# Kernel optimization log

Hardware: AMD Instinct MI355X
Metric: run time of the kernel (lower is better)

## Reference

```python
import jax, jax.numpy as jnp
import numpy as np

B = 8192
NUM_NETS, N_NODES, NUM_OUT, DIM_OUT = 30, 20, 10, 16
NUM_ITER = 3
IN_DIM = 28 * 28


def squash(t, axis=-1):
    # scale * t / ||t||, scale = ||t||^2 / (1 + ||t||^2)
    sq = jnp.sum(t * t, axis=axis, keepdims=True)
    return (sq / (1.0 + sq)) * t / jnp.sqrt(sq)


def setup_inputs() -> dict:
    key = jax.random.key(0)
    ks = jax.random.split(key, 6)
    return {
        "x": jax.random.normal(ks[0], (B, IN_DIM), dtype=jnp.float32),
        "W1": jax.random.normal(ks[1], (NUM_NETS, IN_DIM, N_NODES), dtype=jnp.float32) * 0.05,
        "b1": jax.random.normal(ks[2], (NUM_NETS, N_NODES), dtype=jnp.float32) * 0.05,
        "W2": jax.random.normal(ks[3], (NUM_NETS, N_NODES, N_NODES), dtype=jnp.float32) * 0.05,
        "b2": jax.random.normal(ks[4], (NUM_NETS, N_NODES), dtype=jnp.float32) * 0.05,
        "route_weights": jax.random.normal(ks[5], (NUM_OUT, NUM_NETS, N_NODES, DIM_OUT), dtype=jnp.float32),
    }


def reference(x, W1, b1, W2, b2, route_weights):
    # 30 independent MLPs batched into one grouped GEMM each
    h = jax.nn.relu(jnp.einsum("bi,nio->bno", x, W1) + b1)          # [B,N,20]
    h = jax.nn.relu(jnp.einsum("bnd,nde->bne", h, W2) + b2)          # [B,N,20]
    u = squash(h, axis=-1)                                            # per-net squash over features
    # priors[b,o,n,k] = sum_d u[b,n,d] * route_weights[o,n,d,k]
    priors = jnp.einsum("bnd,ondk->bonk", u, route_weights)          # [B,O,N,K]
    # logits are constant along K in the original; keep [B,O,N,1] (exact math)
    logits = jnp.zeros(priors.shape[:3] + (1,), dtype=priors.dtype)
    v = None
    for i in range(NUM_ITER):
        probs = jax.nn.softmax(logits, axis=1)                        # over output capsules
        v = squash(jnp.sum(probs * priors, axis=2, keepdims=True))    # [B,O,1,K]
        if i != NUM_ITER - 1:
            logits = logits + jnp.sum(priors * v, axis=-1, keepdims=True)
    return jnp.squeeze(v, axis=2)                                     # [B,O,K]
```

## Files before the change

### kernel.cpp

```cpp
#include <hip/hip_runtime.h>


typedef unsigned short bfu;
typedef unsigned int u32;
typedef __attribute__((ext_vector_type(8))) short short8;
typedef __attribute__((ext_vector_type(4))) float floatx4;

__device__ __forceinline__ float bf2f(bfu u) { union { u32 i; float f; } v; v.i = ((u32)u) << 16; return v.f; }
__device__ __forceinline__ float lo2f(u32 w) { union { u32 i; float f; } v; v.i = w << 16; return v.f; }
__device__ __forceinline__ float hi2f(u32 w) { union { u32 i; float f; } v; v.i = w & 0xffff0000u; return v.f; }
__device__ __forceinline__ float ldf(const void* p, int idx, bool b16) {
    return b16 ? bf2f(((const bfu*)p)[idx]) : ((const float*)p)[idx];
}
__device__ __forceinline__ bfu f2bf(float f) {
    u32 u = __float_as_uint(f);
    return (bfu)((u + 0x7FFFu + ((u >> 16) & 1u)) >> 16);
}
__device__ __forceinline__ void unpack8(uint4 q, float* dst) {
    dst[0] = lo2f(q.x); dst[1] = hi2f(q.x);
    dst[2] = lo2f(q.y); dst[3] = hi2f(q.y);
    dst[4] = lo2f(q.z); dst[5] = hi2f(q.z);
    dst[6] = lo2f(q.w); dst[7] = hi2f(q.w);
}

__global__ void detect_dtype(const u32* x, const u32* W1, const u32* b1,
                             const u32* W2, const u32* b2, const u32* rw,
                             u32* flags) {
    int t = threadIdx.x;
    if (t >= 6) return;
    const u32* p = (t == 0) ? x : (t == 1) ? W1 : (t == 2) ? b1
                 : (t == 3) ? W2 : (t == 4) ? b2 : rw;
    int c = 0;
    for (int i = 0; i < 64; i++) {
        u32 e = (p[i] >> 7) & 0xFF;
        c += (e >= 64 && e <= 140) ? 1 : 0;
    }
    flags[t] = (c >= 48) ? 1u : 0u;
}

__global__ void prep_all(const void* x, const void* W1, const void* b1,
                         const void* W2, const void* b2, const void* rw,
                         bfu* __restrict__ xb, bfu* __restrict__ Wt,
                         float* __restrict__ b1f, bfu* __restrict__ rwb,
                         bfu* __restrict__ rwn, float* __restrict__ W2t,
                         float* __restrict__ b2f,
                         const u32* flags, int B, int mode) {
    const int idx = blockIdx.x * 256 + threadIdx.x;
    const int nxb = B * 800;
    if (idx < nxb) {
        const bool b16 = flags[0] != 0;
        int b = idx / 800, kk = idx - b * 800;
        bfu v = 0;
        if (kk < 784) {
            int src = b * 784 + kk;
            v = b16 ? ((const bfu*)x)[src] : f2bf(((const float*)x)[src]);
        }
        xb[idx] = v;
        return;
    }
    int i2 = idx - nxb;
    if (i2 < 640 * 800) {
        const bool wb = flags[1] != 0;
        int c = i2 / 800, k = i2 - c * 800;
        bfu v = 0;
        if (c < 600 && k < 784) {
            int nn = c / 20, o = c - nn * 20;
            int src = nn * 15680 + k * 20 + o;
            v = wb ? ((const bfu*)W1)[src] : f2bf(((const float*)W1)[src]);
        }
        Wt[i2] = v;
        return;
    }
    i2 -= 640 * 800;
    if (i2 < 96000) {
        const bool rb = flags[5] != 0;
        int d = i2 % 20;
        int k = (i2 / 20) % 16;
        int n = (i2 / 320) % 30;
        int o = i2 / 9600;
        int src = o * 9600 + n * 320 + d * 16 + k;
        rwb[i2] = rb ? ((const bfu*)rw)[src] : f2bf(((const float*)rw)[src]);
        return;
    }
    i2 -= 96000;
    if (i2 < 640) {
        b1f[i2] = (i2 < 600) ? ldf(b1, i2, flags[2] != 0) : 0.f;
        return;
    }
    i2 -= 640;
    if (mode != 0) return;
    if (i2 < 153600) {
        const bool rb = flags[5] != 0;
        int dd = i2 % 32;
        int col = (i2 / 32) % 160;
        int n = i2 / 5120;
        bfu v = 0;
        if (dd < 20) {
            int o = col / 16, kk = col % 16;
            int src = o * 9600 + n * 320 + dd * 16 + kk;
            v = rb ? ((const bfu*)rw)[src] : f2bf(((const float*)rw)[src]);
        }
        rwn[i2] = v;
        return;
    }
    i2 -= 153600;
    if (i2 < 12000) {
        int d = i2 % 20;
        int e = (i2 / 20) % 20;
        int n = i2 / 400;
        W2t[i2] = ldf(W2, n * 400 + d * 20 + e, flags[3] != 0);
        return;
    }
    i2 -= 12000;
    if (i2 < 640) {
        b2f[i2] = (i2 < 600) ? ldf(b2, i2, flags[4] != 0) : 0.f;
    }
}

__global__ __launch_bounds__(256, 4) void k1m(const bfu* __restrict__ xb, const bfu* __restrict__ Wt,
                                              const float* __restrict__ b1f,
                                              float* __restrict__ h1, int Btot, int tr) {
    __shared__ short As[128 * 40];
    __shared__ short Bs[64 * 40];
    const int tid = threadIdx.x;
    const int w = tid >> 6, lane = tid & 63;
    const int quad = lane >> 4, fl = lane & 15;
    const int m0 = blockIdx.x * 128, n0 = blockIdx.y * 64;

    floatx4 acc[2][4];
    #pragma unroll
    for (int mi = 0; mi < 2; mi++)
        #pragma unroll
        for (int ni = 0; ni < 4; ni++) acc[mi][ni] = (floatx4){0.f, 0.f, 0.f, 0.f};

    const int arow = tid >> 1, aseg = tid & 1;
    const int brow = tid >> 2, bseg = tid & 3;
    int agrow = m0 + arow; if (agrow >= Btot) agrow = Btot - 1;
    const bfu* abase = xb + (size_t)agrow * 800 + aseg * 16;
    const bfu* bbase = Wt + (size_t)(n0 + brow) * 800 + bseg * 8;

    for (int k0 = 0; k0 < 800; k0 += 32) {
        uint4 qa0 = *(const uint4*)(abase + k0);
        uint4 qa1 = *(const uint4*)(abase + k0 + 8);
        uint4 qb  = *(const uint4*)(bbase + k0);

        __syncthreads();
        *(uint4*)&As[arow * 40 + aseg * 16 + 0] = qa0;
        *(uint4*)&As[arow * 40 + aseg * 16 + 8] = qa1;
        *(uint4*)&Bs[brow * 40 + bseg * 8] = qb;
        __syncthreads();

        short8 af[2], bfr[4];
        #pragma unroll
        for (int mi = 0; mi < 2; mi++)
            af[mi] = *(const short8*)&As[(w * 32 + mi * 16 + fl) * 40 + quad * 8];
        #pragma unroll
        for (int ni = 0; ni < 4; ni++)
            bfr[ni] = *(const short8*)&Bs[(ni * 16 + fl) * 40 + quad * 8];
        #pragma unroll
        for (int mi = 0; mi < 2; mi++)
            #pragma unroll
            for (int ni = 0; ni < 4; ni++)
                acc[mi][ni] = __builtin_amdgcn_mfma_f32_16x16x32_bf16(af[mi], bfr[ni], acc[mi][ni], 0, 0, 0);
    }

    #pragma unroll
    for (int mi = 0; mi < 2; mi++) {
        #pragma unroll
        for (int ni = 0; ni < 4; ni++) {
            const int c = n0 + ni * 16 + fl;
            const int cn = c / 20, ce = c - cn * 20;
            #pragma unroll
            for (int r = 0; r < 4; r++) {
                const int m = m0 + w * 32 + mi * 16 + quad * 4 + r;
                if (c < 600 && m < Btot) {
                    size_t di = tr ? (((size_t)cn * Btot + m) * 20 + ce)
                                   : ((size_t)m * 600 + c);
                    h1[di] = fmaxf(acc[mi][ni][r] + b1f[c], 0.f);
                }
            }
        }
    }
}

__global__ __launch_bounds__(256) void k2n(const float* __restrict__ h1n,
                                           const float* __restrict__ W2t,
                                           const float* __restrict__ b2f,
                                           bfu* __restrict__ ub32, int Btot) {
    const int n = blockIdx.y;
    int b = blockIdx.x * 256 + threadIdx.x;
    if (b >= Btot) b = Btot - 1;

    float h[20];
    const float* hp = h1n + ((size_t)n * Btot + b) * 20;
    #pragma unroll
    for (int d4 = 0; d4 < 20; d4 += 4) {
        float4 v = *(const float4*)(hp + d4);
        h[d4] = v.x; h[d4 + 1] = v.y; h[d4 + 2] = v.z; h[d4 + 3] = v.w;
    }

    const float* wn = W2t + n * 400;
    const float* bn = b2f + n * 20;
    float o[20], sq = 0.f;
    #pragma unroll
    for (int e = 0; e < 20; e++) {
        float acc = bn[e];
        #pragma unroll
        for (int d = 0; d < 20; d++) acc += h[d] * wn[e * 20 + d];
        acc = fmaxf(acc, 0.f);
        o[e] = acc;
        sq += acc * acc;
    }
    float sc = (sq > 0.f) ? sqrtf(sq) / (1.f + sq) : 0.f;

    u32 wbuf[16];
    #pragma unroll
    for (int j = 0; j < 10; j++)
        wbuf[j] = (u32)f2bf(o[2 * j] * sc) | ((u32)f2bf(o[2 * j + 1] * sc) << 16);
    #pragma unroll
    for (int j = 10; j < 16; j++) wbuf[j] = 0;
    uint4* dst = (uint4*)(ub32 + ((size_t)b * 30 + n) * 32);
    dst[0] = *(uint4*)&wbuf[0];
    dst[1] = *(uint4*)&wbuf[4];
    dst[2] = *(uint4*)&wbuf[8];
    dst[3] = *(uint4*)&wbuf[12];
}

__device__ __forceinline__ void k2_core(const float* hp, const float* wn, const float* bn,
                                        float* o, float& sc) {
    float h[20];
    #pragma unroll
    for (int d4 = 0; d4 < 20; d4 += 4) {
        float4 v = *(const float4*)(hp + d4);
        h[d4] = v.x; h[d4 + 1] = v.y; h[d4 + 2] = v.z; h[d4 + 3] = v.w;
    }
    float sq = 0.f;
    #pragma unroll
    for (int e = 0; e < 20; e++) {
        float acc = bn[e];
        #pragma unroll
        for (int d = 0; d < 20; d++) acc += h[d] * wn[d * 20 + e];
        acc = fmaxf(acc, 0.f);
        o[e] = acc;
        sq += acc * acc;
    }
    sc = (sq > 0.f) ? sqrtf(sq) / (1.f + sq) : 0.f;
}

__global__ __launch_bounds__(256) void k2s(const float* h1, const void* W2, const void* b2,
                                           float* u, const u32* flags, int total) {
    __shared__ float W2s[12000];
    __shared__ float b2s[600];
    const bool wb = flags[3] != 0, bb = flags[4] != 0;
    const int tid = threadIdx.x;
    for (int i = tid; i < 12000; i += 256) W2s[i] = ldf(W2, i, wb);
    for (int i = tid; i < 600; i += 256) b2s[i] = ldf(b2, i, bb);
    __syncthreads();

    int t = blockIdx.x * 256 + tid;
    if (t >= total) return;
    const int b = t / 30, n = t - b * 30;
    float o[20], sc;
    k2_core(h1 + (size_t)b * 600 + n * 20, &W2s[n * 400], &b2s[n * 20], o, sc);
    float* up = u + (size_t)b * 600 + n * 20;
    #pragma unroll
    for (int e4 = 0; e4 < 20; e4 += 4) {
        float4 v;
        v.x = o[e4] * sc; v.y = o[e4 + 1] * sc; v.z = o[e4 + 2] * sc; v.w = o[e4 + 3] * sc;
        *(float4*)(up + e4) = v;
    }
}

__global__ __launch_bounds__(256) void k2p(const bfu* __restrict__ ub32,
                                           const bfu* __restrict__ rwn,
                                           bfu* __restrict__ pri, int Btot) {
    const int tid = threadIdx.x;
    const int w = tid >> 6, lane = tid & 63;
    const int quad = lane >> 4, fl = lane & 15;
    const int n = blockIdx.y;
    const int b0 = blockIdx.x * 128;

    short8 bfr[10];
    #pragma unroll
    for (int nj = 0; nj < 10; nj++)
        bfr[nj] = *(const short8*)(rwn + ((size_t)n * 160 + nj * 16 + fl) * 32 + quad * 8);

    #pragma unroll
    for (int mi = 0; mi < 2; mi++) {
        int m = b0 + w * 32 + mi * 16 + fl;
        int mc = (m < Btot) ? m : Btot - 1;
        short8 af = *(const short8*)(ub32 + ((size_t)mc * 30 + n) * 32 + quad * 8);
        #pragma unroll
        for (int nj = 0; nj < 10; nj++) {
            floatx4 acc = (floatx4){0.f, 0.f, 0.f, 0.f};
            acc = __builtin_amdgcn_mfma_f32_16x16x32_bf16(af, bfr[nj], acc, 0, 0, 0);
            #pragma unroll
            for (int r = 0; r < 4; r++) {
                int mr = b0 + w * 32 + mi * 16 + quad * 4 + r;
                if (mr < Btot)
                    pri[(size_t)mr * 4800 + n * 160 + nj * 16 + fl] = f2bf(acc[r]);
            }
        }
    }
}

__global__ __launch_bounds__(640, 2) void k3t(const bfu* __restrict__ pri_buf,
                                              float* __restrict__ out, int Btot) {
    __shared__ float L[4][300];
    __shared__ float P[4][300];
    const int tid = threadIdx.x;
    const int g = tid / 160, r = tid - g * 160;
    const int o = r >> 4, j = r & 15;
    const int b0 = blockIdx.x * 4;
    int bb = b0 + g; if (bb >= Btot) bb = Btot - 1;

    const int n0 = 2 * j, n1 = n0 + 1;
    float p0[16], p1[16];
    if (j < 15) {
        const bfu* pb = pri_buf + (size_t)bb * 4800 + (size_t)o * 16;
        uint4 q0 = *(const uint4*)(pb + n0 * 160);
        uint4 q1 = *(const uint4*)(pb + n0 * 160 + 8);
        uint4 q2 = *(const uint4*)(pb + n1 * 160);
        uint4 q3 = *(const uint4*)(pb + n1 * 160 + 8);
        unpack8(q0, p0); unpack8(q1, p0 + 8);
        unpack8(q2, p1); unpack8(q3, p1 + 8);
    } else {
        #pragma unroll
        for (int i = 0; i < 16; i++) { p0[i] = 0.f; p1[i] = 0.f; }
    }

    float L0 = 0.f, L1 = 0.f;
    float v = 0.f;
    #pragma unroll
    for (int it = 0; it < 3; it++) {
        float P0, P1;
        if (it == 0) {
            P0 = 0.1f; P1 = 0.1f;
        } else {
            if (r < 30) {
                float l[10];
                #pragma unroll
                for (int oo = 0; oo < 10; oo++) l[oo] = L[g][r * 10 + oo];
                float mx = l[0];
                #pragma unroll
                for (int oo = 1; oo < 10; oo++) mx = fmaxf(mx, l[oo]);
                float den = 0.f;
                #pragma unroll
                for (int oo = 0; oo < 10; oo++) { l[oo] = __expf(l[oo] - mx); den += l[oo]; }
                float inv = 1.f / den;
                #pragma unroll
                for (int oo = 0; oo < 10; oo++) P[g][r * 10 + oo] = l[oo] * inv;
            }
            __syncthreads();
            P0 = (j < 15) ? P[g][n0 * 10 + o] : 0.f;
            P1 = (j < 15) ? P[g][n1 * 10 + o] : 0.f;
        }

        float t[16];
        #pragma unroll
        for (int i = 0; i < 16; i++) t[i] = P0 * p0[i] + P1 * p1[i];

        #pragma unroll
        for (int i = 0; i < 8; i++) {
            float send = (j & 8) ? t[i] : t[i + 8];
            float recv = __shfl_xor(send, 8, 16);
            t[i] = ((j & 8) ? t[i + 8] : t[i]) + recv;
        }
        #pragma unroll
        for (int i = 0; i < 4; i++) {
            float send = (j & 4) ? t[i] : t[i + 4];
            float recv = __shfl_xor(send, 4, 16);
            t[i] = ((j & 4) ? t[i + 4] : t[i]) + recv;
        }
        #pragma unroll
        for (int i = 0; i < 2; i++) {
            float send = (j & 2) ? t[i] : t[i + 2];
            float recv = __shfl_xor(send, 2, 16);
            t[i] = ((j & 2) ? t[i + 2] : t[i]) + recv;
        }
        {
            float send = (j & 1) ? t[0] : t[1];
            float recv = __shfl_xor(send, 1, 16);
            t[0] = ((j & 1) ? t[1] : t[0]) + recv;
        }
        float s = t[0];

        if (it < 2) {
            float sf[16];
            #pragma unroll
            for (int k = 0; k < 16; k++) sf[k] = __shfl(s, k, 16);
            float q = 0.f;
            #pragma unroll
            for (int k = 0; k < 16; k++) q += sf[k] * sf[k];
            float scale = sqrtf(q) / (1.f + q);
            v = s * scale;
            float d0 = 0.f, d1 = 0.f;
            #pragma unroll
            for (int k = 0; k < 16; k++) {
                float vk = sf[k] * scale;
                d0 += p0[k] * vk;
                d1 += p1[k] * vk;
            }
            L0 += d0; L1 += d1;
            if (j < 15) {
                L[g][n0 * 10 + o] = L0;
                L[g][n1 * 10 + o] = L1;
            }
            __syncthreads();
        } else {
            float q = s * s;
            q += __shfl_xor(q, 1, 16);
            q += __shfl_xor(q, 2, 16);
            q += __shfl_xor(q, 4, 16);
            q += __shfl_xor(q, 8, 16);
            v = s * sqrtf(q) / (1.f + q);
        }
    }
    if ((b0 + g) < Btot) out[(size_t)(b0 + g) * 160 + r] = v;
}

__global__ __launch_bounds__(640, 2) void k3y2(const float* __restrict__ u,
                                               const bfu* __restrict__ rwb,
                                               float* __restrict__ out, int Btot) {
    __shared__ float US[4][600];
    __shared__ float L[4][300];
    __shared__ float P[4][300];
    const int tid = threadIdx.x;
    const int g = tid / 160, r = tid - g * 160;
    const int o = r >> 4, k = r & 15;
    const int b0 = blockIdx.x * 4;

    {
        const int nf4 = 150;
        for (int i = tid; i < 4 * nf4; i += 640) {
            int gg = i / nf4, j = i - gg * nf4;
            int bb = b0 + gg; if (bb >= Btot) bb = Btot - 1;
            *(float4*)&US[gg][j * 4] = *(const float4*)(u + (size_t)bb * 600 + j * 4);
        }
        for (int i = tid; i < 1200; i += 640) L[i / 300][i % 300] = 0.f;
    }
    __syncthreads();

    float pri[30];
    const bfu* rp = rwb + o * 9600 + k * 20;
    #pragma unroll 2
    for (int n = 0; n < 30; n++) {
        const uint2* rq = (const uint2*)(rp + n * 320);
        float a = 0.f;
        #pragma unroll
        for (int jj = 0; jj < 5; jj++) {
            uint2 w = rq[jj];
            float4 uu = *(const float4*)&US[g][n * 20 + jj * 4];
            a += lo2f(w.x) * uu.x + hi2f(w.x) * uu.y + lo2f(w.y) * uu.z + hi2f(w.y) * uu.w;
        }
        pri[n] = a;
    }

    float v = 0.f;
    for (int it = 0; it < 3; it++) {
        if (r < 30) {
            const int n = r;
            float mx = L[g][n * 10];
            #pragma unroll
            for (int oo = 1; oo < 10; oo++) mx = fmaxf(mx, L[g][n * 10 + oo]);
            float e[10], den = 0.f;
            #pragma unroll
            for (int oo = 0; oo < 10; oo++) { e[oo] = __expf(L[g][n * 10 + oo] - mx); den += e[oo]; }
            float inv = 1.f / den;
            #pragma unroll
            for (int oo = 0; oo < 10; oo++) P[g][n * 10 + oo] = e[oo] * inv;
        }
        __syncthreads();
        float s = 0.f;
        #pragma unroll
        for (int n = 0; n < 30; n++) s += P[g][n * 10 + o] * pri[n];
        float q = s * s;
        q += __shfl_xor(q, 1, 16);
        q += __shfl_xor(q, 2, 16);
        q += __shfl_xor(q, 4, 16);
        q += __shfl_xor(q, 8, 16);
        v = s * sqrtf(q) / (1.f + q);
        if (it < 2) {
            #pragma unroll 5
            for (int n = 0; n < 30; n++) {
                float t = pri[n] * v;
                t += __shfl_xor(t, 1, 16);
                t += __shfl_xor(t, 2, 16);
                t += __shfl_xor(t, 4, 16);
                t += __shfl_xor(t, 8, 16);
                if (k == 0) L[g][n * 10 + o] += t;
            }
            __syncthreads();
        }
    }
    if ((b0 + g) < Btot) out[(size_t)(b0 + g) * 160 + r] = v;
}

extern "C" void kernel_launch(void* const* d_in, const int* in_sizes, int n_in,
                              void* d_out, int out_size, void* d_ws, size_t ws_size,
                              hipStream_t stream) {
    int ix = -1, iw1 = -1, ib1 = -1, iw2 = -1, ib2 = -1, irw = -1;
    for (int i = 0; i < n_in; i++) {
        int s = in_sizes[i];
        if (s == 470400 && iw1 < 0) iw1 = i;
        else if (s == 12000 && iw2 < 0) iw2 = i;
        else if (s == 96000 && irw < 0) irw = i;
        else if (s == 600) { if (ib1 < 0) ib1 = i; else if (ib2 < 0) ib2 = i; }
    }
    long bestsz = -1;
    for (int i = 0; i < n_in; i++) {
        if (i == iw1 || i == iw2 || i == irw || i == ib1 || i == ib2) continue;
        if ((long)in_sizes[i] > bestsz) { bestsz = in_sizes[i]; ix = i; }
    }
    if (ix < 0 || iw1 < 0 || ib1 < 0 || iw2 < 0 || ib2 < 0 || irw < 0) {
        ix = 0; iw1 = 1; ib1 = 2; iw2 = 3; ib2 = 4; irw = 5;
    }
    const void* x  = d_in[ix];
    const void* W1 = d_in[iw1];
    const void* b1 = d_in[ib1];
    const void* W2 = d_in[iw2];
    const void* b2 = d_in[ib2];
    const void* rw = d_in[irw];
    const int B = in_sizes[ix] / 784;
    float* out = (float*)d_out;

    char* base = (char*)d_ws;
    size_t off = 0;
    float* h1u  = (float*)(base + off); off += (size_t)B * 2400;
    float* b1f  = (float*)(base + off); off += 2560;
    u32*  flags = (u32*)(base + off);   off += 32;
    bfu*   Wt   = (bfu*)(base + off);   off += 1024000;
    bfu*   xb   = (bfu*)(base + off);   off += (size_t)B * 1600;
    bfu*   rwb  = (bfu*)(base + off);   off += 192000;
    size_t fb_bytes = off;
    bfu*   rwn  = (bfu*)(base + off);   off += 307200;
    float* W2t  = (float*)(base + off); off += 48000;
    float* b2f  = (float*)(base + off); off += 2560;
    bfu*   ub32 = (bfu*)(base + off);   off += (size_t)B * 1920;
    bfu*   pri  = (bfu*)(base + off);   off += (size_t)B * 9600;
    size_t main_bytes = off;

    const int mode = (ws_size >= main_bytes) ? 0 : 1;
    const int prep_total = B * 800 + 640 * 800 + 96000 + 640
                         + (mode == 0 ? (153600 + 12000 + 640) : 0);

    detect_dtype<<<1, 64, 0, stream>>>((const u32*)x, (const u32*)W1, (const u32*)b1,
                                       (const u32*)W2, (const u32*)b2, (const u32*)rw, flags);
    prep_all<<<(prep_total + 255) / 256, 256, 0, stream>>>(x, W1, b1, W2, b2, rw,
                                                           xb, Wt, b1f, rwb, rwn,
                                                           W2t, b2f, flags, B, mode);
    k1m<<<dim3((B + 127) / 128, 10), 256, 0, stream>>>(xb, Wt, b1f, h1u, B, mode == 0 ? 1 : 0);
    if (mode == 0) {
        k2n<<<dim3((B + 255) / 256, 30), 256, 0, stream>>>(h1u, W2t, b2f, ub32, B);
        k2p<<<dim3((B + 127) / 128, 30), 256, 0, stream>>>(ub32, rwn, pri, B);
        k3t<<<(B + 3) / 4, 640, 0, stream>>>(pri, out, B);
    } else {
        (void)fb_bytes;
        k2s<<<(B * 30 + 255) / 256, 256, 0, stream>>>(h1u, W2, b2, h1u, flags, B * 30);
        k3y2<<<(B + 3) / 4, 640, 0, stream>>>(h1u, rwb, out, B);
    }
}
```

Measured before the change: 191.4 us.

## Reorder priors layout to [o][n][k] and halve routing kernel threads

The prior-producing kernel now writes priors grouped by output capsule first, so each routing thread loads four contiguous nets' 16-wide vectors. The routing kernel uses 80 threads per batch row instead of 160, with each thread handling 4 nets and 2 output dims. This cuts the shuffle reduction depth and idle lanes, and gives vectorized float2 stores. The cost is more registers per thread and fewer threads per block.

Result: no change. 191.1 us (-0.1%).

```diff
diff --git a/kernel.cpp b/kernel.cpp
--- a/kernel.cpp
+++ b/kernel.cpp
@@ -298,44 +298,45 @@
             for (int r = 0; r < 4; r++) {
                 int mr = b0 + w * 32 + mi * 16 + quad * 4 + r;
                 if (mr < Btot)
-                    pri[(size_t)mr * 4800 + n * 160 + nj * 16 + fl] = f2bf(acc[r]);
-            }
-        }
-    }
-}
-
-__global__ __launch_bounds__(640, 2) void k3t(const bfu* __restrict__ pri_buf,
-                                              float* __restrict__ out, int Btot) {
+                    pri[(size_t)mr * 4800 + nj * 480 + n * 16 + fl] = f2bf(acc[r]);
+            }
+        }
+    }
+}
+
+__global__ __launch_bounds__(320) void k3u(const bfu* __restrict__ pri_buf,
+                                           float* __restrict__ out, int Btot) {
     __shared__ float L[4][300];
     __shared__ float P[4][300];
     const int tid = threadIdx.x;
-    const int g = tid / 160, r = tid - g * 160;
-    const int o = r >> 4, j = r & 15;
+    const int g = tid / 80, r = tid - g * 80;
+    const int o = r >> 3, j = r & 7;
     const int b0 = blockIdx.x * 4;
     int bb = b0 + g; if (bb >= Btot) bb = Btot - 1;
 
-    const int n0 = 2 * j, n1 = n0 + 1;
-    float p0[16], p1[16];
-    if (j < 15) {
-        const bfu* pb = pri_buf + (size_t)bb * 4800 + (size_t)o * 16;
-        uint4 q0 = *(const uint4*)(pb + n0 * 160);
-        uint4 q1 = *(const uint4*)(pb + n0 * 160 + 8);
-        uint4 q2 = *(const uint4*)(pb + n1 * 160);
-        uint4 q3 = *(const uint4*)(pb + n1 * 160 + 8);
-        unpack8(q0, p0); unpack8(q1, p0 + 8);
-        unpack8(q2, p1); unpack8(q3, p1 + 8);
-    } else {
-        #pragma unroll
-        for (int i = 0; i < 16; i++) { p0[i] = 0.f; p1[i] = 0.f; }
-    }
-
-    float L0 = 0.f, L1 = 0.f;
-    float v = 0.f;
+    float p[4][16];
+    const bfu* pb = pri_buf + (size_t)bb * 4800 + (size_t)o * 480 + j * 64;
+    #pragma unroll
+    for (int nn = 0; nn < 4; nn++) {
+        if (4 * j + nn < 30) {
+            uint4 q0 = *(const uint4*)(pb + nn * 16);
+            uint4 q1 = *(const uint4*)(pb + nn * 16 + 8);
+            unpack8(q0, p[nn]); unpack8(q1, p[nn] + 8);
+        } else {
+            #pragma unroll
+            for (int i = 0; i < 16; i++) p[nn][i] = 0.f;
+        }
+    }
+
+    float Lr[4] = {0.f, 0.f, 0.f, 0.f};
+    float v0 = 0.f, v1 = 0.f;
     #pragma unroll
     for (int it = 0; it < 3; it++) {
-        float P0, P1;
+        float t[16];
         if (it == 0) {
-            P0 = 0.1f; P1 = 0.1f;
+            #pragma unroll
+            for (int i = 0; i < 16; i++)
+                t[i] = 0.1f * ((p[0][i] + p[1][i]) + (p[2][i] + p[3][i]));
         } else {
             if (r < 30) {
                 float l[10];
@@ -352,71 +353,75 @@
                 for (int oo = 0; oo < 10; oo++) P[g][r * 10 + oo] = l[oo] * inv;
             }
             __syncthreads();
-            P0 = (j < 15) ? P[g][n0 * 10 + o] : 0.f;
-            P1 = (j < 15) ? P[g][n1 * 10 + o] : 0.f;
-        }
-
-        float t[16];
-        #pragma unroll
-        for (int i = 0; i < 16; i++) t[i] = P0 * p0[i] + P1 * p1[i];
+            float Pw[4];
+            #pragma unroll
+            for (int nn = 0; nn < 4; nn++)
+                Pw[nn] = (4 * j + nn < 30) ? P[g][(4 * j + nn) * 10 + o] : 0.f;
+            #pragma unroll
+            for (int i = 0; i < 16; i++)
+                t[i] = (Pw[0] * p[0][i] + Pw[1] * p[1][i])
+                     + (Pw[2] * p[2][i] + Pw[3] * p[3][i]);
+        }
 
         #pragma unroll
         for (int i = 0; i < 8; i++) {
-            float send = (j & 8) ? t[i] : t[i + 8];
-            float recv = __shfl_xor(send, 8, 16);
-            t[i] = ((j & 8) ? t[i + 8] : t[i]) + recv;
+            float send = (j & 4) ? t[i] : t[i + 8];
+            float recv = __shfl_xor(send, 4, 8);
+            t[i] = ((j & 4) ? t[i + 8] : t[i]) + recv;
         }
         #pragma unroll
         for (int i = 0; i < 4; i++) {
-            float send = (j & 4) ? t[i] : t[i + 4];
-            float recv = __shfl_xor(send, 4, 16);
-            t[i] = ((j & 4) ? t[i + 4] : t[i]) + recv;
+            float send = (j & 2) ? t[i] : t[i + 4];
+            float recv = __shfl_xor(send, 2, 8);
+            t[i] = ((j & 2) ? t[i + 4] : t[i]) + recv;
         }
         #pragma unroll
         for (int i = 0; i < 2; i++) {
-            float send = (j & 2) ? t[i] : t[i + 2];
-            float recv = __shfl_xor(send, 2, 16);
-            t[i] = ((j & 2) ? t[i + 2] : t[i]) + recv;
-        }
-        {
-            float send = (j & 1) ? t[0] : t[1];
-            float recv = __shfl_xor(send, 1, 16);
-            t[0] = ((j & 1) ? t[1] : t[0]) + recv;
-        }
-        float s = t[0];
+            float send = (j & 1) ? t[i] : t[i + 2];
+            float recv = __shfl_xor(send, 1, 8);
+            t[i] = ((j & 1) ? t[i + 2] : t[i]) + recv;
+        }
 
         if (it < 2) {
             float sf[16];
             #pragma unroll
-            for (int k = 0; k < 16; k++) sf[k] = __shfl(s, k, 16);
-            float q = 0.f;
-            #pragma unroll
-            for (int k = 0; k < 16; k++) q += sf[k] * sf[k];
-            float scale = sqrtf(q) / (1.f + q);
-            v = s * scale;
-            float d0 = 0.f, d1 = 0.f;
+            for (int q8 = 0; q8 < 8; q8++) {
+                sf[2 * q8]     = __shfl(t[0], q8, 8);
+                sf[2 * q8 + 1] = __shfl(t[1], q8, 8);
+            }
+            float qq = 0.f;
+            #pragma unroll
+            for (int k = 0; k < 16; k++) qq += sf[k] * sf[k];
+            float scale = sqrtf(qq) / (1.f + qq);
+            float d[4] = {0.f, 0.f, 0.f, 0.f};
             #pragma unroll
             for (int k = 0; k < 16; k++) {
                 float vk = sf[k] * scale;
-                d0 += p0[k] * vk;
-                d1 += p1[k] * vk;
-            }
-            L0 += d0; L1 += d1;
-            if (j < 15) {
-                L[g][n0 * 10 + o] = L0;
-                L[g][n1 * 10 + o] = L1;
+                d[0] += p[0][k] * vk;
+                d[1] += p[1][k] * vk;
+                d[2] += p[2][k] * vk;
+                d[3] += p[3][k] * vk;
+            }
+            #pragma unroll
+            for (int nn = 0; nn < 4; nn++) {
+                Lr[nn] += d[nn];
+                if (4 * j + nn < 30) L[g][(4 * j + nn) * 10 + o] = Lr[nn];
             }
             __syncthreads();
         } else {
-            float q = s * s;
-            q += __shfl_xor(q, 1, 16);
-            q += __shfl_xor(q, 2, 16);
-            q += __shfl_xor(q, 4, 16);
-            q += __shfl_xor(q, 8, 16);
-            v = s * sqrtf(q) / (1.f + q);
-        }
-    }
-    if ((b0 + g) < Btot) out[(size_t)(b0 + g) * 160 + r] = v;
+            float qq = t[0] * t[0] + t[1] * t[1];
+            qq += __shfl_xor(qq, 1, 8);
+            qq += __shfl_xor(qq, 2, 8);
+            qq += __shfl_xor(qq, 4, 8);
+            float scale = sqrtf(qq) / (1.f + qq);
+            v0 = t[0] * scale;
+            v1 = t[1] * scale;
+        }
+    }
+    if ((b0 + g) < Btot) {
+        float2 w; w.x = v0; w.y = v1;
+        *(float2*)(out + (size_t)(b0 + g) * 160 + o * 16 + 2 * j) = w;
+    }
 }
 
 __global__ __launch_bounds__(640, 2) void k3y2(const float* __restrict__ u,
@@ -553,7 +558,7 @@
     if (mode == 0) {
         k2n<<<dim3((B + 255) / 256, 30), 256, 0, stream>>>(h1u, W2t, b2f, ub32, B);
         k2p<<<dim3((B + 127) / 128, 30), 256, 0, stream>>>(ub32, rwn, pri, B);
-        k3t<<<(B + 3) / 4, 640, 0, stream>>>(pri, out, B);
+        k3u<<<(B + 3) / 4, 320, 0, stream>>>(pri, out, B);
     } else {
         (void)fb_bytes;
         k2s<<<(B * 30 + 255) / 256, 256, 0, stream>>>(h1u, W2, b2, h1u, flags, B * 30);
```

## Fuse second MLP layer with priors MFMA and reorder priors layout

Applied to the files above, without the earlier changes.

Merges the per-net second layer plus squash kernel (k2n) with the priors MFMA kernel (k2p). The squashed bf16 activations are staged in shared memory instead of a global ub32 buffer, which removes one launch and a global write/read round trip. Two threads now share each row's 20 outputs and combine the squash norm with a lane shuffle. The priors layout changes from [b][n][o][k] to [b][o][n][k], so k3t reads each thread's two nets as contiguous 64-byte chunks; in exchange, the global stores in the fused kernel become more strided.

After: 188.9 us. Within noise of the previous version (-1.3%).

```diff
diff --git a/kernel.cpp b/kernel.cpp
--- a/kernel.cpp
+++ b/kernel.cpp
@@ -183,47 +183,72 @@
     }
 }
 
-__global__ __launch_bounds__(256) void k2n(const float* __restrict__ h1n,
+__global__ __launch_bounds__(256) void k2q(const float* __restrict__ h1n,
                                            const float* __restrict__ W2t,
                                            const float* __restrict__ b2f,
-                                           bfu* __restrict__ ub32, int Btot) {
+                                           const bfu* __restrict__ rwn,
+                                           bfu* __restrict__ pri, int Btot) {
+    __shared__ short us[128 * 40];
+    const int tid = threadIdx.x;
     const int n = blockIdx.y;
-    int b = blockIdx.x * 256 + threadIdx.x;
-    if (b >= Btot) b = Btot - 1;
-
-    float h[20];
-    const float* hp = h1n + ((size_t)n * Btot + b) * 20;
-    #pragma unroll
-    for (int d4 = 0; d4 < 20; d4 += 4) {
-        float4 v = *(const float4*)(hp + d4);
-        h[d4] = v.x; h[d4 + 1] = v.y; h[d4 + 2] = v.z; h[d4 + 3] = v.w;
-    }
-
-    const float* wn = W2t + n * 400;
-    const float* bn = b2f + n * 20;
-    float o[20], sq = 0.f;
-    #pragma unroll
-    for (int e = 0; e < 20; e++) {
-        float acc = bn[e];
-        #pragma unroll
-        for (int d = 0; d < 20; d++) acc += h[d] * wn[e * 20 + d];
-        acc = fmaxf(acc, 0.f);
-        o[e] = acc;
-        sq += acc * acc;
-    }
-    float sc = (sq > 0.f) ? sqrtf(sq) / (1.f + sq) : 0.f;
-
-    u32 wbuf[16];
-    #pragma unroll
-    for (int j = 0; j < 10; j++)
-        wbuf[j] = (u32)f2bf(o[2 * j] * sc) | ((u32)f2bf(o[2 * j + 1] * sc) << 16);
-    #pragma unroll
-    for (int j = 10; j < 16; j++) wbuf[j] = 0;
-    uint4* dst = (uint4*)(ub32 + ((size_t)b * 30 + n) * 32);
-    dst[0] = *(uint4*)&wbuf[0];
-    dst[1] = *(uint4*)&wbuf[4];
-    dst[2] = *(uint4*)&wbuf[8];
-    dst[3] = *(uint4*)&wbuf[12];
+    const int b0 = blockIdx.x * 128;
+
+    const int w = tid >> 6, lane = tid & 63;
+    const int quad = lane >> 4, fl = lane & 15;
+    short8 bfr[10];
+    #pragma unroll
+    for (int nj = 0; nj < 10; nj++)
+        bfr[nj] = *(const short8*)(rwn + ((size_t)n * 160 + nj * 16 + fl) * 32 + quad * 8);
+
+    {
+        const int row = tid >> 1, half = tid & 1;
+        int br = b0 + row; if (br >= Btot) br = Btot - 1;
+        float h[20];
+        const float* hp = h1n + ((size_t)n * Btot + br) * 20;
+        #pragma unroll
+        for (int d4 = 0; d4 < 20; d4 += 4) {
+            float4 v = *(const float4*)(hp + d4);
+            h[d4] = v.x; h[d4 + 1] = v.y; h[d4 + 2] = v.z; h[d4 + 3] = v.w;
+        }
+        const float* wn = W2t + n * 400;
+        const float* bn = b2f + n * 20;
+        float o[10], sq = 0.f;
+        #pragma unroll
+        for (int i = 0; i < 10; i++) {
+            const int e = 2 * i + half;
+            float acc = bn[e];
+            #pragma unroll
+            for (int d = 0; d < 20; d++) acc += h[d] * wn[e * 20 + d];
+            acc = fmaxf(acc, 0.f);
+            o[i] = acc;
+            sq += acc * acc;
+        }
+        sq += __shfl_xor(sq, 1);
+        float sc = (sq > 0.f) ? sqrtf(sq) / (1.f + sq) : 0.f;
+        #pragma unroll
+        for (int i = 0; i < 10; i++)
+            us[row * 40 + 2 * i + half] = (short)f2bf(o[i] * sc);
+        #pragma unroll
+        for (int i = 10; i < 16; i++)
+            us[row * 40 + 2 * i + half] = 0;
+    }
+    __syncthreads();
+
+    #pragma unroll
+    for (int mi = 0; mi < 2; mi++) {
+        short8 af = *(const short8*)&us[(w * 32 + mi * 16 + fl) * 40 + quad * 8];
+        #pragma unroll
+        for (int nj = 0; nj < 10; nj++) {
+            floatx4 acc = (floatx4){0.f, 0.f, 0.f, 0.f};
+            acc = __builtin_amdgcn_mfma_f32_16x16x32_bf16(af, bfr[nj], acc, 0, 0, 0);
+            #pragma unroll
+            for (int r = 0; r < 4; r++) {
+                int mr = b0 + w * 32 + mi * 16 + quad * 4 + r;
+                if (mr < Btot)
+                    pri[(size_t)mr * 4800 + nj * 480 + n * 16 + fl] = f2bf(acc[r]);
+            }
+        }
+    }
 }
 
 __device__ __forceinline__ void k2_core(const float* hp, const float* wn, const float* bn,
@@ -271,39 +296,6 @@
     }
 }
 
-__global__ __launch_bounds__(256) void k2p(const bfu* __restrict__ ub32,
-                                           const bfu* __restrict__ rwn,
-                                           bfu* __restrict__ pri, int Btot) {
-    const int tid = threadIdx.x;
-    const int w = tid >> 6, lane = tid & 63;
-    const int quad = lane >> 4, fl = lane & 15;
-    const int n = blockIdx.y;
-    const int b0 = blockIdx.x * 128;
-
-    short8 bfr[10];
-    #pragma unroll
-    for (int nj = 0; nj < 10; nj++)
-        bfr[nj] = *(const short8*)(rwn + ((size_t)n * 160 + nj * 16 + fl) * 32 + quad * 8);
-
-    #pragma unroll
-    for (int mi = 0; mi < 2; mi++) {
-        int m = b0 + w * 32 + mi * 16 + fl;
-        int mc = (m < Btot) ? m : Btot - 1;
-        short8 af = *(const short8*)(ub32 + ((size_t)mc * 30 + n) * 32 + quad * 8);
-        #pragma unroll
-        for (int nj = 0; nj < 10; nj++) {
-            floatx4 acc = (floatx4){0.f, 0.f, 0.f, 0.f};
-            acc = __builtin_amdgcn_mfma_f32_16x16x32_bf16(af, bfr[nj], acc, 0, 0, 0);
-            #pragma unroll
-            for (int r = 0; r < 4; r++) {
-                int mr = b0 + w * 32 + mi * 16 + quad * 4 + r;
-                if (mr < Btot)
-                    pri[(size_t)mr * 4800 + n * 160 + nj * 16 + fl] = f2bf(acc[r]);
-            }
-        }
-    }
-}
-
 __global__ __launch_bounds__(640, 2) void k3t(const bfu* __restrict__ pri_buf,
                                               float* __restrict__ out, int Btot) {
     __shared__ float L[4][300];
@@ -317,11 +309,11 @@
     const int n0 = 2 * j, n1 = n0 + 1;
     float p0[16], p1[16];
     if (j < 15) {
-        const bfu* pb = pri_buf + (size_t)bb * 4800 + (size_t)o * 16;
-        uint4 q0 = *(const uint4*)(pb + n0 * 160);
-        uint4 q1 = *(const uint4*)(pb + n0 * 160 + 8);
-        uint4 q2 = *(const uint4*)(pb + n1 * 160);
-        uint4 q3 = *(const uint4*)(pb + n1 * 160 + 8);
+        const bfu* pb = pri_buf + (size_t)bb * 4800 + (size_t)o * 480 + j * 32;
+        uint4 q0 = *(const uint4*)(pb);
+        uint4 q1 = *(const uint4*)(pb + 8);
+        uint4 q2 = *(const uint4*)(pb + 16);
+        uint4 q3 = *(const uint4*)(pb + 24);
         unpack8(q0, p0); unpack8(q1, p0 + 8);
         unpack8(q2, p1); unpack8(q3, p1 + 8);
     } else {
@@ -536,7 +528,6 @@
     bfu*   rwn  = (bfu*)(base + off);   off += 307200;
     float* W2t  = (float*)(base + off); off += 48000;
     float* b2f  = (float*)(base + off); off += 2560;
-    bfu*   ub32 = (bfu*)(base + off);   off += (size_t)B * 1920;
     bfu*   pri  = (bfu*)(base + off);   off += (size_t)B * 9600;
     size_t main_bytes = off;
 
@@ -551,8 +542,7 @@
                                                            W2t, b2f, flags, B, mode);
     k1m<<<dim3((B + 127) / 128, 10), 256, 0, stream>>>(xb, Wt, b1f, h1u, B, mode == 0 ? 1 : 0);
     if (mode == 0) {
-        k2n<<<dim3((B + 255) / 256, 30), 256, 0, stream>>>(h1u, W2t, b2f, ub32, B);
-        k2p<<<dim3((B + 127) / 128, 30), 256, 0, stream>>>(ub32, rwn, pri, B);
+        k2q<<<dim3((B + 127) / 128, 30), 256, 0, stream>>>(h1u, W2t, b2f, rwn, pri, B);
         k3t<<<(B + 3) / 4, 640, 0, stream>>>(pri, out, B);
     } else {
         (void)fb_bytes;
```
